# Kernel tuning notes

Hardware: AMD Instinct MI355X
Metric: run time of the kernel (lower is better)

The kernel has to match this reference:

```python
import jax, jax.numpy as jnp
import numpy as np

N = 20000      # num nodes
E = 320000     # num edges (avg degree 16)
R = 8          # num relations
D = 256        # input_dim / hidden dim
L = 6          # num_layers
EE = 32        # edge_embed_dim
B = 64         # batch size
K = 32         # num_negative + 1


def _layer_norm(x, g, b, eps=1e-5):
    mu = jnp.mean(x, axis=-1, keepdims=True)
    var = jnp.var(x, axis=-1, keepdims=True)
    return (x - mu) * jax.lax.rsqrt(var + eps) * g + b


def setup_inputs() -> dict:
    key = jax.random.key(0)
    ks = jax.random.split(key, 10)
    edge_index = jax.random.randint(ks[0], (2, E), 0, N)
    edge_type = jax.random.randint(ks[1], (E,), 0, R)
    edge_embed = jax.random.normal(ks[2], (E, EE), dtype=jnp.float32)
    src = jax.random.randint(ks[3], (B, K), 0, N)
    tgt = jax.random.randint(ks[4], (B, K), 0, N)
    rel = jax.random.randint(ks[5], (B, K), 0, R)
    batch = jnp.stack([src, tgt, rel], axis=-1)  # [B, K, 3]
    s = 1.0 / np.sqrt(D)
    W = jax.random.normal(ks[6], (L, R, D, D), dtype=jnp.float32) * s      # per-relation weights
    Wself = jax.random.normal(ks[7], (L, D, D), dtype=jnp.float32) * s     # self-loop weights
    We = jax.random.normal(ks[8], (L, EE, D), dtype=jnp.float32) * (1.0 / np.sqrt(EE))  # edge-embed proj (stage add)
    gamma = jnp.ones((L, D), dtype=jnp.float32)
    beta = jnp.zeros((L, D), dtype=jnp.float32)
    rel_emb = jax.random.normal(ks[9], (R, D), dtype=jnp.float32) * s      # DistMult relation embedding
    return dict(edge_index=edge_index, edge_type=edge_type, edge_embed=edge_embed,
                batch=batch, W=W, Wself=Wself, We=We, gamma=gamma, beta=beta,
                rel_emb=rel_emb)


def reference(edge_index, edge_type, edge_embed, batch, W, Wself, We, gamma, beta, rel_emb):
    src, dst = edge_index[0], edge_index[1]
    # mean aggregation denominator: in-degree per node (over all relations)
    deg = jnp.clip(jax.ops.segment_sum(jnp.ones((E,), jnp.float32), dst, num_segments=N), 1.0)
    # segment id combining relation and destination node -> aggregate-then-transform trick
    seg = edge_type * N + dst
    x = jnp.ones((N, D), dtype=jnp.float32)
    for l in range(L):
        # stage 'add': message = x[src] + proj(edge_embed)
        msg = x[src] + edge_embed @ We[l]                                  # [E, D]
        agg = jax.ops.segment_sum(msg, seg, num_segments=R * N).reshape(R, N, D)
        h = jnp.einsum('rnd,rdf->nf', agg, W[l]) / deg[:, None] + x @ Wself[l]
        h = jax.nn.relu(_layer_norm(h, gamma[l], beta[l]))
        x = h + x  # short_cut residual
    # DistMult scoring: gather source/target/relation embeddings, mul, sum
    s_emb = x[batch[..., 0]]          # [B, K, D]
    t_emb = x[batch[..., 1]]          # [B, K, D]
    r_emb = rel_emb[batch[..., 2]]    # [B, K, D]
    return jnp.sum(s_emb * r_emb * t_emb, axis=-1)  # [B, K]
```

## Files before the change

kernel.cpp:

```cpp
#include <hip/hip_runtime.h>
#include <hip/hip_bf16.h>

#define NN 20000
#define NP 20080
#define NE 320000
#define RR 8
#define DD 256
#define LL 6
#define EED 32
#define BB 64
#define KK 32
#define MM (NN * RR)
#define NSB 79
#define BMR 80
#define NGB 251
#define YROW 2304
#define YROWB 4608
#define HSTR 260

typedef __bf16 bf8 __attribute__((ext_vector_type(8)));
typedef float f4 __attribute__((ext_vector_type(4)));

__device__ inline float lo2f(unsigned v) { return __uint_as_float(v << 16); }
__device__ inline float hi2f(unsigned v) { return __uint_as_float(v & 0xffff0000u); }
__device__ inline unsigned short f2bf(float f) {
    unsigned u = __float_as_uint(f);
    return (unsigned short)((u + 0x7fff + ((u >> 16) & 1)) >> 16);
}
__device__ inline unsigned pack2(float lo, float hi) {
    return (unsigned)f2bf(lo) | ((unsigned)f2bf(hi) << 16);
}

#define GLOAD_LDS16(src, dst)                                                  \
    __builtin_amdgcn_global_load_lds(                                          \
        (const __attribute__((address_space(1))) unsigned int*)(src),          \
        (__attribute__((address_space(3))) unsigned int*)(dst), 16, 0, 0)

#define LGKM_BARRIER()                                                         \
    do {                                                                       \
        __builtin_amdgcn_sched_barrier(0);                                     \
        asm volatile("s_waitcnt lgkmcnt(0)");                                  \
        __builtin_amdgcn_s_barrier();                                          \
        __builtin_amdgcn_sched_barrier(0);                                     \
    } while (0)


__global__ __launch_bounds__(256) void hist_kernel(const int* __restrict__ dstv,
                                                   const int* __restrict__ typev,
                                                   int* __restrict__ hist) {
    int e = blockIdx.x * 256 + threadIdx.x;
    if (e < NE) atomicAdd(&hist[dstv[e] * 8 + typev[e]], 1);
}

__global__ __launch_bounds__(256) void scan1_kernel(const int* __restrict__ hist,
                                                    int* __restrict__ excl,
                                                    int* __restrict__ bsums) {
    __shared__ int tmp[256];
    int tid = threadIdx.x;
    int base = blockIdx.x * 2048 + tid * 8;
    int v[8]; int s = 0;
#pragma unroll
    for (int i = 0; i < 8; ++i) {
        v[i] = (base + i < MM) ? hist[base + i] : 0;
        s += v[i];
    }
    tmp[tid] = s;
    __syncthreads();
    for (int off = 1; off < 256; off <<= 1) {
        int t = (tid >= off) ? tmp[tid - off] : 0;
        __syncthreads();
        tmp[tid] += t;
        __syncthreads();
    }
    int run = tmp[tid] - s;
#pragma unroll
    for (int i = 0; i < 8; ++i) {
        if (base + i < MM) excl[base + i] = run;
        run += v[i];
    }
    if (tid == 255) bsums[blockIdx.x] = tmp[255];
}

__global__ __launch_bounds__(128) void scan2_kernel(int* __restrict__ bsums) {
    __shared__ int tmp[128];
    int tid = threadIdx.x;
    int orig = (tid < NSB) ? bsums[tid] : 0;
    tmp[tid] = orig;
    __syncthreads();
    for (int off = 1; off < 128; off <<= 1) {
        int t = (tid >= off) ? tmp[tid - off] : 0;
        __syncthreads();
        tmp[tid] += t;
        __syncthreads();
    }
    if (tid < NSB) bsums[tid] = tmp[tid] - orig;
}

__global__ __launch_bounds__(256) void add_off_kernel(const int* __restrict__ excl,
                                                      const int* __restrict__ bsums,
                                                      int* __restrict__ seg_start,
                                                      int* __restrict__ cursor) {
    int i = blockIdx.x * 256 + threadIdx.x;
    if (i < MM) {
        int v = excl[i] + bsums[i >> 11];
        seg_start[i] = v;
        cursor[i] = v;
    }
    if (i == 0) seg_start[MM] = NE;
}

__global__ __launch_bounds__(256) void sort_scatter_kernel(
    const int* __restrict__ srcv, const int* __restrict__ dstv,
    const int* __restrict__ typev, int* __restrict__ cursor,
    int* __restrict__ esrcY, int* __restrict__ eid) {
    int e = blockIdx.x * 256 + threadIdx.x;
    if (e < NE) {
        int key = dstv[e] * 8 + typev[e];
        int pos = atomicAdd(&cursor[key], 1);
        esrcY[pos] = srcv[e] * YROWB + typev[e] * 512;
        eid[pos]   = e;
    }
}

__global__ __launch_bounds__(256) void invdeg_kernel(const int* __restrict__ seg_start,
                                                     float* __restrict__ invdeg) {
    int i = blockIdx.x * 256 + threadIdx.x;
    if (i < NN) {
        int d = seg_start[i * 8 + 8] - seg_start[i * 8];
        invdeg[i] = 1.0f / (float)max(d, 1);
    }
}


__global__ __launch_bounds__(256) void eagg_kernel(
    const int* __restrict__ seg_start, const int* __restrict__ eid,
    const float* __restrict__ ee, const float* __restrict__ invdeg,
    unsigned short* __restrict__ eaggbf) {
    int tid = threadIdx.x;
    int s = blockIdx.x * 8 + (tid >> 5);
    int j = tid & 31;
    int n = s >> 3, r = s & 7;
    int j0 = seg_start[s], j1 = seg_start[s + 1];
    float sum = 0.0f;
#pragma unroll 1
    for (int p = j0; p < j1; p += 4) {
        int rem = j1 - p;
        int e4[4];
        float fv[4];
#pragma unroll
        for (int t = 0; t < 4; ++t)
            e4[t] = eid[(t < rem) ? p + t : p];
#pragma unroll
        for (int t = 0; t < 4; ++t)
            fv[t] = ee[(size_t)e4[t] * EED + j];
#pragma unroll
        for (int t = 0; t < 4; ++t)
            sum += (t < rem) ? fv[t] : 0.0f;
    }
    eaggbf[(size_t)n * DD + r * EED + j] = f2bf(sum * invdeg[n]);
}

__global__ __launch_bounds__(256) void whe_kernel(const float* __restrict__ We,
                                                  const float* __restrict__ W,
                                                  float* __restrict__ Whe) {
    __shared__ float WeS[EED * 32];
    int b = blockIdx.x;
    int l = b >> 6;
    int r = (b >> 3) & 7;
    int dc = b & 7;
    int tid = threadIdx.x;
    {
        int j = tid >> 3, dl = (tid & 7) * 4;
        *(float4*)&WeS[j * 32 + dl] =
            *(const float4*)&We[(size_t)l * EED * DD + (size_t)j * DD + dc * 32 + dl];
    }
    __syncthreads();
    const float* Wr = W + ((size_t)l * 8 + r) * DD * DD + (size_t)dc * 32 * DD;
    float acc[EED];
#pragma unroll
    for (int j = 0; j < EED; ++j) acc[j] = 0.0f;
    for (int dl = 0; dl < 32; ++dl) {
        float w = Wr[(size_t)dl * DD + tid];
#pragma unroll
        for (int j = 0; j < EED; ++j) acc[j] += WeS[j * 32 + dl] * w;
    }
    float* outp = Whe + (size_t)l * DD * DD + r * EED * DD + tid;
#pragma unroll
    for (int j = 0; j < EED; ++j) unsafeAtomicAdd(&outp[j * DD], acc[j]);
}

__global__ __launch_bounds__(256) void bswz_kernel(const float* __restrict__ W,
                                                   const float* __restrict__ Wself,
                                                   const float* __restrict__ Whe,
                                                   unsigned short* __restrict__ Bsw) {
    int gid = blockIdx.x * 256 + threadIdx.x;
    int f = gid & 255;
    int t = gid >> 8;
    int quad = t & 3; t >>= 2;
    int kb = t & 7; t >>= 3;
    int p = t % 10, l = t / 10;
    const float* base = (p <= 7) ? W + ((size_t)l * 8 + p) * DD * DD
                      : (p == 8) ? Wself + (size_t)l * DD * DD
                                 : Whe + (size_t)l * DD * DD;
    int k0 = kb * 32 + quad * 8;
    unsigned pk[4];
#pragma unroll
    for (int jj = 0; jj < 4; ++jj)
        pk[jj] = pack2(base[(size_t)(k0 + 2 * jj) * DD + f],
                       base[(size_t)(k0 + 2 * jj + 1) * DD + f]);
    uint4 v = make_uint4(pk[0], pk[1], pk[2], pk[3]);
    *(uint4*)&Bsw[(size_t)gid * 8] = v;
}

__global__ __launch_bounds__(256) void init_x_kernel(float* __restrict__ xA,
                                                     float* __restrict__ xB,
                                                     unsigned short* __restrict__ xbfA,
                                                     unsigned short* __restrict__ xbfB) {
    int i = blockIdx.x * 256 + threadIdx.x;
    ((float4*)xA)[i] = make_float4(1.f, 1.f, 1.f, 1.f);
    ((float4*)xB)[i] = make_float4(1.f, 1.f, 1.f, 1.f);
    ((uint2*)xbfA)[i] = make_uint2(0x3f803f80u, 0x3f803f80u);
    ((uint2*)xbfB)[i] = make_uint2(0x3f803f80u, 0x3f803f80u);
}

__global__ __launch_bounds__(512) void ymm_kernel(
    const unsigned short* __restrict__ xbfin, const unsigned short* __restrict__ eaggbf,
    const unsigned short* __restrict__ Bswl, unsigned short* __restrict__ Y,
    unsigned short* __restrict__ etermb) {
    __shared__ __align__(16) unsigned char smem[40960 + BMR * HSTR * 4];
    unsigned char* As = smem;
    float* Hs = (float*)(smem + 40960);
    int tid = threadIdx.x;
    int wv = tid >> 6, lane = tid & 63;
    int row0 = blockIdx.x * BMR;
    int m = lane & 15, quad = lane >> 4;

#pragma unroll
    for (int i = 0; i < 5; ++i) {
        int bc = i * 512 + wv * 64;
        int c = bc + lane;
        int row = c >> 5, sc = c & 31, scs = sc ^ (row & 31);
        GLOAD_LDS16(xbfin + (size_t)(row0 + row) * DD + scs * 8, As + (size_t)c * 16);
    }
    bf8 breg[2][2];
#pragma unroll
    for (int nt = 0; nt < 2; ++nt) {
        breg[0][nt] = *(const bf8*)&Bswl[((size_t)quad * 256 + wv * 32 + nt * 16 + m) * 8];
        breg[1][nt] = *(const bf8*)&Bswl[(((size_t)4 + quad) * 256 + wv * 32 + nt * 16 + m) * 8];
    }
    __syncthreads();

#pragma unroll 1
    for (int rt = 0; rt < 10; ++rt) {
        if (rt == 9) {
            __syncthreads();
#pragma unroll
            for (int i = 0; i < 5; ++i) {
                int bc = i * 512 + wv * 64;
                int c = bc + lane;
                int row = c >> 5, sc = c & 31, scs = sc ^ (row & 31);
                GLOAD_LDS16(eaggbf + (size_t)(row0 + row) * DD + scs * 8, As + (size_t)c * 16);
            }
            __syncthreads();
        }
        f4 acc[5][2] = {};
#pragma unroll
        for (int kb = 0; kb < 8; ++kb) {
            bf8 afr[5];
#pragma unroll
            for (int mt = 0; mt < 5; ++mt) {
                int rowl = mt * 16 + m;
                afr[mt] = *(bf8*)&As[rowl * 512 + (((kb * 4 + quad) ^ (rowl & 31)) * 16)];
            }
#pragma unroll
            for (int mt = 0; mt < 5; ++mt)
#pragma unroll
                for (int nt = 0; nt < 2; ++nt)
                    acc[mt][nt] = __builtin_amdgcn_mfma_f32_16x16x32_bf16(
                        afr[mt], breg[kb & 1][nt], acc[mt][nt], 0, 0, 0);
            int gn = rt * 8 + kb + 2;
            if (gn < 80) {
#pragma unroll
                for (int nt = 0; nt < 2; ++nt)
                    breg[kb & 1][nt] = *(const bf8*)&Bswl[((size_t)gn * 4 + quad) * 2048
                                                          + ((size_t)(wv * 32 + nt * 16 + m)) * 8];
            }
        }
        if (rt > 0) LGKM_BARRIER();
#pragma unroll
        for (int mt = 0; mt < 5; ++mt)
#pragma unroll
            for (int nt = 0; nt < 2; ++nt)
#pragma unroll
                for (int rg = 0; rg < 4; ++rg)
                    Hs[(mt * 16 + quad * 4 + rg) * HSTR + wv * 32 + nt * 16 + m] = acc[mt][nt][rg];
        LGKM_BARRIER();
        unsigned short* outb = (rt < 9) ? Y : etermb;
        size_t ostride = (rt < 9) ? YROW : DD;
        int colOff = (rt < 9) ? rt * 256 : 0;
#pragma unroll
        for (int c2 = 0; c2 < 10; ++c2) {
            int li = c2 * 512 + tid;
            int row = li >> 6, u4 = li & 63;
            float4 v = *(float4*)&Hs[row * HSTR + u4 * 4];
            *(uint2*)&outb[(size_t)(row0 + row) * ostride + colOff + u4 * 4] =
                make_uint2(pack2(v.x, v.y), pack2(v.z, v.w));
        }
    }
}

__global__ __launch_bounds__(512) void aggln_kernel(
    const int* __restrict__ seg_start, const int* __restrict__ esrcY,
    const unsigned short* __restrict__ Y, const unsigned short* __restrict__ eterml,
    const float* __restrict__ xin, const float* __restrict__ gl,
    const float* __restrict__ bl, float* __restrict__ xout,
    unsigned short* __restrict__ xbfout) {
    int tid = threadIdx.x;
    int wv = tid >> 6, lane = tid & 63;
    int n = blockIdx.x * 8 + wv;
    float4 g  = *(const float4*)&gl[lane * 4];
    float4 bb = *(const float4*)&bl[lane * 4];
    int j0 = seg_start[n * 8], j1 = seg_start[n * 8 + 8];
    float idg = 1.0f / (float)max(j1 - j0, 1);
    const char* Yb = (const char*)Y;
    size_t lo8 = (size_t)(lane * 8);
    float a0 = 0.f, a1 = 0.f, a2 = 0.f, a3 = 0.f;
#pragma unroll 1
    for (int j = j0; j < j1; j += 16) {
        int rem = j1 - j;
        uint2 gvv[16];
#pragma unroll
        for (int t = 0; t < 16; ++t) {
            int jj = (t < rem) ? j + t : j;
            gvv[t] = *(const uint2*)(Yb + (size_t)(unsigned)esrcY[jj] + lo8);
        }
#pragma unroll
        for (int t = 0; t < 16; ++t) {
            unsigned vx = (t < rem) ? gvv[t].x : 0u;
            unsigned vy = (t < rem) ? gvv[t].y : 0u;
            a0 += lo2f(vx); a1 += hi2f(vx);
            a2 += lo2f(vy); a3 += hi2f(vy);
        }
    }
    uint2 sv = *(const uint2*)(Yb + (size_t)n * YROWB + 4096 + lo8);
    uint2 ev = *(const uint2*)&eterml[(size_t)n * DD + lane * 4];
    float h0 = a0 * idg + lo2f(sv.x) + lo2f(ev.x);
    float h1 = a1 * idg + hi2f(sv.x) + hi2f(ev.x);
    float h2 = a2 * idg + lo2f(sv.y) + lo2f(ev.y);
    float h3 = a3 * idg + hi2f(sv.y) + hi2f(ev.y);
    float s = h0 + h1 + h2 + h3;
    float q = h0 * h0 + h1 * h1 + h2 * h2 + h3 * h3;
#pragma unroll
    for (int off = 32; off; off >>= 1) {
        s += __shfl_xor(s, off);
        q += __shfl_xor(q, off);
    }
    float mu  = s * (1.0f / DD);
    float var = q * (1.0f / DD) - mu * mu;
    float rs  = rsqrtf(var + 1e-5f);
    size_t xi = (size_t)n * DD + lane * 4;
    float4 xv = *(const float4*)&xin[xi];
    float4 o;
    o.x = fmaxf((h0 - mu) * rs * g.x + bb.x, 0.0f) + xv.x;
    o.y = fmaxf((h1 - mu) * rs * g.y + bb.y, 0.0f) + xv.y;
    o.z = fmaxf((h2 - mu) * rs * g.z + bb.z, 0.0f) + xv.z;
    o.w = fmaxf((h3 - mu) * rs * g.w + bb.w, 0.0f) + xv.w;
    *(float4*)&xout[xi] = o;
    *(uint2*)&xbfout[xi] = make_uint2(pack2(o.x, o.y), pack2(o.z, o.w));
}

__global__ __launch_bounds__(256) void score_kernel(
    const int* __restrict__ batch, const float* __restrict__ x,
    const float* __restrict__ rel_emb, float* __restrict__ out) {
    int tid = threadIdx.x;
    int wave = tid >> 6, lane = tid & 63;
    int idx = blockIdx.x * 4 + wave;
    int s = batch[idx * 3 + 0], t = batch[idx * 3 + 1], r = batch[idx * 3 + 2];
    float4 sv = *(const float4*)&x[(size_t)s * DD + lane * 4];
    float4 tv = *(const float4*)&x[(size_t)t * DD + lane * 4];
    float4 rv = *(const float4*)&rel_emb[(size_t)r * DD + lane * 4];
    float sum = sv.x * rv.x * tv.x + sv.y * rv.y * tv.y +
                sv.z * rv.z * tv.z + sv.w * rv.w * tv.w;
#pragma unroll
    for (int off = 32; off; off >>= 1) sum += __shfl_xor(sum, off);
    if (lane == 0) out[idx] = sum;
}

extern "C" void kernel_launch(void* const* d_in, const int* in_sizes, int n_in,
                              void* d_out, int out_size, void* d_ws, size_t ws_size,
                              hipStream_t stream) {
    const int*   edge_index = (const int*)d_in[0];
    const int*   srcv   = edge_index;
    const int*   dstv   = edge_index + NE;
    const int*   typev  = (const int*)d_in[1];
    const float* ee     = (const float*)d_in[2];
    const int*   batch  = (const int*)d_in[3];
    const float* W      = (const float*)d_in[4];
    const float* Wself  = (const float*)d_in[5];
    const float* We     = (const float*)d_in[6];
    const float* gamma  = (const float*)d_in[7];
    const float* beta   = (const float*)d_in[8];
    const float* rel_emb= (const float*)d_in[9];
    float* out = (float*)d_out;

    float* xA     = (float*)d_ws;
    float* xB     = xA + (size_t)NP * DD;
    float* Whe    = xB + (size_t)NP * DD;
    float* invdeg = Whe + (size_t)LL * DD * DD;
    unsigned short* xbfA   = (unsigned short*)(invdeg + NN);
    unsigned short* xbfB   = xbfA + (size_t)NP * DD;
    unsigned short* eaggbf = xbfB + (size_t)NP * DD;
    unsigned short* Bsw    = eaggbf + (size_t)NP * DD;
    int* hist      = (int*)(Bsw + (size_t)LL * 2560 * DD);
    int* excl      = hist + MM;
    int* seg_start = excl + MM;
    int* cursor    = seg_start + MM + 1;
    int* bsums     = cursor + MM;
    int* esrcY     = bsums + 256;
    int* eid       = esrcY + NE;
    unsigned short* etermb =
        (unsigned short*)(((uintptr_t)(eid + NE) + 255) & ~(uintptr_t)255);
    unsigned short* Y = etermb + (size_t)NP * DD;

    hipMemsetAsync(hist, 0, MM * sizeof(int), stream);
    hist_kernel<<<(NE + 255) / 256, 256, 0, stream>>>(dstv, typev, hist);
    scan1_kernel<<<NSB, 256, 0, stream>>>(hist, excl, bsums);
    scan2_kernel<<<1, 128, 0, stream>>>(bsums);
    add_off_kernel<<<(MM + 255) / 256, 256, 0, stream>>>(excl, bsums, seg_start, cursor);
    invdeg_kernel<<<(NN + 255) / 256, 256, 0, stream>>>(seg_start, invdeg);
    sort_scatter_kernel<<<(NE + 255) / 256, 256, 0, stream>>>(srcv, dstv, typev, cursor, esrcY, eid);

    eagg_kernel<<<MM / 8, 256, 0, stream>>>(seg_start, eid, ee, invdeg, eaggbf);
    hipMemsetAsync(Whe, 0, (size_t)LL * DD * DD * sizeof(float), stream);
    whe_kernel<<<LL * 64, 256, 0, stream>>>(We, W, Whe);
    bswz_kernel<<<LL * 10 * 8 * 4, 256, 0, stream>>>(W, Wself, Whe, Bsw);
    init_x_kernel<<<(NP * DD / 4) / 256, 256, 0, stream>>>(xA, xB, xbfA, xbfB);

    float* xin = xA;  float* xout = xB;
    unsigned short* xbin = xbfA;  unsigned short* xbout = xbfB;
    for (int l = 0; l < LL; ++l) {
        const unsigned short* Bl = Bsw + (size_t)l * 2560 * DD;
        ymm_kernel<<<NGB, 512, 0, stream>>>(xbin, eaggbf, Bl, Y, etermb);
        aggln_kernel<<<NN / 8, 512, 0, stream>>>(seg_start, esrcY, Y, etermb,
            xin, gamma + (size_t)l * DD, beta + (size_t)l * DD, xout, xbout);
        float* t = xin; xin = xout; xout = t;
        unsigned short* tb = xbin; xbin = xbout; xbout = tb;
    }
    score_kernel<<<(BB * KK) / 4, 256, 0, stream>>>(batch, xin, rel_emb, out);
}
```

Measured before the change: 772.0 us.

## Precompute edge-term GEMM for all layers in one kernel, widen stores

The edge-embedding term GEMM depends only on the aggregated edge embeddings and the weights, not on x. It moves out of the per-layer ymm kernel into a single eterm6 kernel that computes all six layers up front into a larger buffer. The per-layer GEMM drops from ten row tiles to nine, no longer reloads a second A tile, and writes 16-byte nontemporal stores. aggln now issues its self/eterm/x loads before the gather loop and writes its outputs nontemporally. The cost is six times the eterm buffer and one extra launch, and the eterm work stays on the critical path.

After: 830.1 us. +7.5%, slower.

```diff
diff --git a/kernel.cpp b/kernel.cpp
--- a/kernel.cpp
+++ b/kernel.cpp
@@ -20,6 +20,7 @@
 
 typedef __bf16 bf8 __attribute__((ext_vector_type(8)));
 typedef float f4 __attribute__((ext_vector_type(4)));
+typedef unsigned int u32x4 __attribute__((ext_vector_type(4)));
 
 __device__ inline float lo2f(unsigned v) { return __uint_as_float(v << 16); }
 __device__ inline float hi2f(unsigned v) { return __uint_as_float(v & 0xffff0000u); }
@@ -223,10 +224,86 @@
     ((uint2*)xbfB)[i] = make_uint2(0x3f803f80u, 0x3f803f80u);
 }
 
+__global__ __launch_bounds__(512) void eterm6_kernel(
+    const unsigned short* __restrict__ eaggbf, const unsigned short* __restrict__ Bsw,
+    unsigned short* __restrict__ etermb6) {
+    __shared__ __align__(16) unsigned char smem[40960 + BMR * HSTR * 4];
+    unsigned char* As = smem;
+    float* Hs = (float*)(smem + 40960);
+    int tid = threadIdx.x;
+    int wv = tid >> 6, lane = tid & 63;
+    int row0 = blockIdx.x * BMR;
+    int m = lane & 15, quad = lane >> 4;
+    int col = wv * 32 + m;
+
+#pragma unroll
+    for (int i = 0; i < 5; ++i) {
+        int bc = i * 512 + wv * 64;
+        int c = bc + lane;
+        int row = c >> 5, sc = c & 31, scs = sc ^ (row & 31);
+        GLOAD_LDS16(eaggbf + (size_t)(row0 + row) * DD + scs * 8, As + (size_t)c * 16);
+    }
+    __syncthreads();
+
+#pragma unroll 1
+    for (int l = 0; l < LL; ++l) {
+        const unsigned short* Bswl = Bsw + (size_t)l * 2560 * DD;
+        bf8 breg[2][2];
+#pragma unroll
+        for (int nt = 0; nt < 2; ++nt) {
+            breg[0][nt] = *(const bf8*)&Bswl[(((size_t)72 * 4 + quad) * 256 + col + nt * 16) * 8];
+            breg[1][nt] = *(const bf8*)&Bswl[(((size_t)73 * 4 + quad) * 256 + col + nt * 16) * 8];
+        }
+        f4 acc[5][2] = {};
+#pragma unroll
+        for (int kb = 0; kb < 8; ++kb) {
+            bf8 afr[5];
+#pragma unroll
+            for (int mt = 0; mt < 5; ++mt) {
+                int rowl = mt * 16 + m;
+                afr[mt] = *(bf8*)&As[rowl * 512 + (((kb * 4 + quad) ^ (rowl & 31)) * 16)];
+            }
+#pragma unroll
+            for (int mt = 0; mt < 5; ++mt)
+#pragma unroll
+                for (int nt = 0; nt < 2; ++nt)
+                    acc[mt][nt] = __builtin_amdgcn_mfma_f32_16x16x32_bf16(
+                        afr[mt], breg[kb & 1][nt], acc[mt][nt], 0, 0, 0);
+            int gn = 72 + kb + 2;
+            if (gn < 80) {
+#pragma unroll
+                for (int nt = 0; nt < 2; ++nt)
+                    breg[kb & 1][nt] = *(const bf8*)&Bswl[((size_t)gn * 4 + quad) * 2048
+                                                          + ((size_t)(col + nt * 16)) * 8];
+            }
+        }
+        if (l > 0) LGKM_BARRIER();
+#pragma unroll
+        for (int mt = 0; mt < 5; ++mt)
+#pragma unroll
+            for (int nt = 0; nt < 2; ++nt)
+#pragma unroll
+                for (int rg = 0; rg < 4; ++rg)
+                    Hs[(mt * 16 + quad * 4 + rg) * HSTR + wv * 32 + nt * 16 + m] = acc[mt][nt][rg];
+        LGKM_BARRIER();
+        unsigned short* outl = etermb6 + (size_t)l * NP * DD;
+#pragma unroll
+        for (int c2 = 0; c2 < 5; ++c2) {
+            int li = c2 * 512 + tid;
+            int row = li >> 5, u8 = li & 31;
+            float4 va = *(float4*)&Hs[row * HSTR + u8 * 8];
+            float4 vb = *(float4*)&Hs[row * HSTR + u8 * 8 + 4];
+            u32x4 pv = {pack2(va.x, va.y), pack2(va.z, va.w),
+                        pack2(vb.x, vb.y), pack2(vb.z, vb.w)};
+            __builtin_nontemporal_store(pv,
+                (u32x4*)&outl[(size_t)(row0 + row) * DD + u8 * 8]);
+        }
+    }
+}
+
 __global__ __launch_bounds__(512) void ymm_kernel(
-    const unsigned short* __restrict__ xbfin, const unsigned short* __restrict__ eaggbf,
-    const unsigned short* __restrict__ Bswl, unsigned short* __restrict__ Y,
-    unsigned short* __restrict__ etermb) {
+    const unsigned short* __restrict__ xbfin, const unsigned short* __restrict__ Bswl,
+    unsigned short* __restrict__ Y) {
     __shared__ __align__(16) unsigned char smem[40960 + BMR * HSTR * 4];
     unsigned char* As = smem;
     float* Hs = (float*)(smem + 40960);
@@ -251,18 +328,7 @@
     __syncthreads();
 
 #pragma unroll 1
-    for (int rt = 0; rt < 10; ++rt) {
-        if (rt == 9) {
-            __syncthreads();
-#pragma unroll
-            for (int i = 0; i < 5; ++i) {
-                int bc = i * 512 + wv * 64;
-                int c = bc + lane;
-                int row = c >> 5, sc = c & 31, scs = sc ^ (row & 31);
-                GLOAD_LDS16(eaggbf + (size_t)(row0 + row) * DD + scs * 8, As + (size_t)c * 16);
-            }
-            __syncthreads();
-        }
+    for (int rt = 0; rt < 9; ++rt) {
         f4 acc[5][2] = {};
 #pragma unroll
         for (int kb = 0; kb < 8; ++kb) {
@@ -279,7 +345,7 @@
                     acc[mt][nt] = __builtin_amdgcn_mfma_f32_16x16x32_bf16(
                         afr[mt], breg[kb & 1][nt], acc[mt][nt], 0, 0, 0);
             int gn = rt * 8 + kb + 2;
-            if (gn < 80) {
+            if (gn < 72) {
 #pragma unroll
                 for (int nt = 0; nt < 2; ++nt)
                     breg[kb & 1][nt] = *(const bf8*)&Bswl[((size_t)gn * 4 + quad) * 2048
@@ -295,16 +361,16 @@
                 for (int rg = 0; rg < 4; ++rg)
                     Hs[(mt * 16 + quad * 4 + rg) * HSTR + wv * 32 + nt * 16 + m] = acc[mt][nt][rg];
         LGKM_BARRIER();
-        unsigned short* outb = (rt < 9) ? Y : etermb;
-        size_t ostride = (rt < 9) ? YROW : DD;
-        int colOff = (rt < 9) ? rt * 256 : 0;
-#pragma unroll
-        for (int c2 = 0; c2 < 10; ++c2) {
+#pragma unroll
+        for (int c2 = 0; c2 < 5; ++c2) {
             int li = c2 * 512 + tid;
-            int row = li >> 6, u4 = li & 63;
-            float4 v = *(float4*)&Hs[row * HSTR + u4 * 4];
-            *(uint2*)&outb[(size_t)(row0 + row) * ostride + colOff + u4 * 4] =
-                make_uint2(pack2(v.x, v.y), pack2(v.z, v.w));
+            int row = li >> 5, u8 = li & 31;
+            float4 va = *(float4*)&Hs[row * HSTR + u8 * 8];
+            float4 vb = *(float4*)&Hs[row * HSTR + u8 * 8 + 4];
+            u32x4 pv = {pack2(va.x, va.y), pack2(va.z, va.w),
+                        pack2(vb.x, vb.y), pack2(vb.z, vb.w)};
+            __builtin_nontemporal_store(pv,
+                (u32x4*)&Y[(size_t)(row0 + row) * YROW + rt * 256 + u8 * 8]);
         }
     }
 }
@@ -318,12 +384,16 @@
     int tid = threadIdx.x;
     int wv = tid >> 6, lane = tid & 63;
     int n = blockIdx.x * 8 + wv;
-    float4 g  = *(const float4*)&gl[lane * 4];
-    float4 bb = *(const float4*)&bl[lane * 4];
     int j0 = seg_start[n * 8], j1 = seg_start[n * 8 + 8];
     float idg = 1.0f / (float)max(j1 - j0, 1);
     const char* Yb = (const char*)Y;
     size_t lo8 = (size_t)(lane * 8);
+    size_t xi = (size_t)n * DD + lane * 4;
+    uint2 sv = *(const uint2*)(Yb + (size_t)n * YROWB + 4096 + lo8);
+    uint2 ev = *(const uint2*)&eterml[(size_t)n * DD + lane * 4];
+    float4 xv = *(const float4*)&xin[xi];
+    float4 g  = *(const float4*)&gl[lane * 4];
+    float4 bb = *(const float4*)&bl[lane * 4];
     float a0 = 0.f, a1 = 0.f, a2 = 0.f, a3 = 0.f;
 #pragma unroll 1
     for (int j = j0; j < j1; j += 16) {
@@ -342,8 +412,6 @@
             a2 += lo2f(vy); a3 += hi2f(vy);
         }
     }
-    uint2 sv = *(const uint2*)(Yb + (size_t)n * YROWB + 4096 + lo8);
-    uint2 ev = *(const uint2*)&eterml[(size_t)n * DD + lane * 4];
     float h0 = a0 * idg + lo2f(sv.x) + lo2f(ev.x);
     float h1 = a1 * idg + hi2f(sv.x) + hi2f(ev.x);
     float h2 = a2 * idg + lo2f(sv.y) + lo2f(ev.y);
@@ -358,15 +426,15 @@
     float mu  = s * (1.0f / DD);
     float var = q * (1.0f / DD) - mu * mu;
     float rs  = rsqrtf(var + 1e-5f);
-    size_t xi = (size_t)n * DD + lane * 4;
-    float4 xv = *(const float4*)&xin[xi];
-    float4 o;
-    o.x = fmaxf((h0 - mu) * rs * g.x + bb.x, 0.0f) + xv.x;
-    o.y = fmaxf((h1 - mu) * rs * g.y + bb.y, 0.0f) + xv.y;
-    o.z = fmaxf((h2 - mu) * rs * g.z + bb.z, 0.0f) + xv.z;
-    o.w = fmaxf((h3 - mu) * rs * g.w + bb.w, 0.0f) + xv.w;
-    *(float4*)&xout[xi] = o;
-    *(uint2*)&xbfout[xi] = make_uint2(pack2(o.x, o.y), pack2(o.z, o.w));
+    f4 o;
+    o[0] = fmaxf((h0 - mu) * rs * g.x + bb.x, 0.0f) + xv.x;
+    o[1] = fmaxf((h1 - mu) * rs * g.y + bb.y, 0.0f) + xv.y;
+    o[2] = fmaxf((h2 - mu) * rs * g.z + bb.z, 0.0f) + xv.z;
+    o[3] = fmaxf((h3 - mu) * rs * g.w + bb.w, 0.0f) + xv.w;
+    __builtin_nontemporal_store(o, (f4*)&xout[xi]);
+    unsigned long long pb = (unsigned long long)pack2(o[0], o[1])
+                          | ((unsigned long long)pack2(o[2], o[3]) << 32);
+    __builtin_nontemporal_store(pb, (unsigned long long*)&xbfout[xi]);
 }
 
 __global__ __launch_bounds__(256) void score_kernel(
@@ -418,9 +486,9 @@
     int* bsums     = cursor + MM;
     int* esrcY     = bsums + 256;
     int* eid       = esrcY + NE;
-    unsigned short* etermb =
+    unsigned short* etermb6 =
         (unsigned short*)(((uintptr_t)(eid + NE) + 255) & ~(uintptr_t)255);
-    unsigned short* Y = etermb + (size_t)NP * DD;
+    unsigned short* Y = etermb6 + (size_t)LL * NP * DD;
 
     hipMemsetAsync(hist, 0, MM * sizeof(int), stream);
     hist_kernel<<<(NE + 255) / 256, 256, 0, stream>>>(dstv, typev, hist);
@@ -435,13 +503,14 @@
     whe_kernel<<<LL * 64, 256, 0, stream>>>(We, W, Whe);
     bswz_kernel<<<LL * 10 * 8 * 4, 256, 0, stream>>>(W, Wself, Whe, Bsw);
     init_x_kernel<<<(NP * DD / 4) / 256, 256, 0, stream>>>(xA, xB, xbfA, xbfB);
+    eterm6_kernel<<<NGB, 512, 0, stream>>>(eaggbf, Bsw, etermb6);
 
     float* xin = xA;  float* xout = xB;
     unsigned short* xbin = xbfA;  unsigned short* xbout = xbfB;
     for (int l = 0; l < LL; ++l) {
-        const unsigned short* Bl = Bsw + (size_t)l * 2560 * DD;
-        ymm_kernel<<<NGB, 512, 0, stream>>>(xbin, eaggbf, Bl, Y, etermb);
-        aggln_kernel<<<NN / 8, 512, 0, stream>>>(seg_start, esrcY, Y, etermb,
+        ymm_kernel<<<NGB, 512, 0, stream>>>(xbin, Bsw + (size_t)l * 2560 * DD, Y);
+        aggln_kernel<<<NN / 8, 512, 0, stream>>>(seg_start, esrcY, Y,
+            etermb6 + (size_t)l * NP * DD,
             xin, gamma + (size_t)l * DD, beta + (size_t)l * DD, xout, xbout);
         float* t = xin; xin = xout; xout = t;
         unsigned short* tb = xbin; xbin = xbout; xbout = tb;
```
